# Kernel tuning notes

Measured on AMD Instinct MI355X. Metric: run time of the kernel, lower is better.

## Reference

```python
import jax, jax.numpy as jnp
import numpy as np

SOBEL_X = jnp.array([[-1., 0., 1.], [-2., 0., 2.], [-1., 0., 1.]], dtype=jnp.float32)
SOBEL_Y = jnp.array([[-1., -2., -1.], [0., 0., 0.], [1., 2., 1.]], dtype=jnp.float32)


def _dwconv(x, k):
    # depthwise 3x3 conv, padding=1, groups=C. x: [B,C,H,W], k: [3,3]
    C = x.shape[1]
    kern = jnp.broadcast_to(k[None, None], (C, 1, 3, 3)).astype(x.dtype)
    return jax.lax.conv_general_dilated(
        x, kern, window_strides=(1, 1), padding=((1, 1), (1, 1)),
        dimension_numbers=('NCHW', 'OIHW', 'NCHW'), feature_group_count=C)


def setup_inputs() -> dict:
    key = jax.random.key(0)
    k1, _ = jax.random.split(key)
    u = jax.random.normal(k1, (16, 3, 512, 512), dtype=jnp.float32)
    theta = jnp.ones((1,), dtype=jnp.float32)
    return {"u": u, "theta": theta}


def reference(u, theta):
    # first derivatives
    ux = _dwconv(u, SOBEL_X)
    uy = _dwconv(u, SOBEL_Y)
    # second derivatives
    uxx = _dwconv(ux, SOBEL_X)
    uxy = _dwconv(ux, SOBEL_Y)
    uyy = _dwconv(uy, SOBEL_Y)
    # Gaussian curvature
    denom = (1.0 + ux * ux + uy * uy) ** 2
    G = (uxx * uyy - uxy * uxy) / (denom + 1e-6)
    # theta * u is computed but unused in the original forward (kept faithful)
    _ = theta * u
    phi_G = jnp.exp(-jnp.abs(G))
    P = phi_G * ux
    Q = phi_G * uy
    div_term = _dwconv(P, SOBEL_X) + _dwconv(Q, SOBEL_Y)
    return u + div_term
```

## Files before the change

kernel.cpp:

```cpp
#include <hip/hip_runtime.h>
#include <math.h>


#define HB   8
#define NROW (HB + 6)
#define NT   256

#define STEP(TT, S0, S1, S2) do {                                              \
    const int Tt = (TT);                                                       \
               \
    const float ur0 = ucen[S0][0], ur1 = ucen[S0][1],                          \
                ur2 = ucen[S0][2], ur3 = ucen[S0][3];                          \
    if (Tt < NROW) {                                                           \
                        \
        const int gy = gy0 + Tt - 3;                                           \
        float* w = uw[S0];                                                     \
        if ((unsigned)gy < (unsigned)H) {                                      \
            const float* row = uc + (long)gy * W;                              \
            const float4 va = *(const float4*)(row + ca);                      \
            const float4 vb = *(const float4*)(row + c0);                      \
            const float4 vc = *(const float4*)(row + cc);                      \
            w[0] = inb0  ? va.x : 0.f;  w[1]  = inb1  ? va.y : 0.f;            \
            w[2] = inb2  ? va.z : 0.f;  w[3]  = inb3  ? va.w : 0.f;            \
            w[4] = vb.x;                w[5]  = vb.y;                          \
            w[6] = vb.z;                w[7]  = vb.w;                          \
            w[8] = inb8  ? vc.x : 0.f;  w[9]  = inb9  ? vc.y : 0.f;            \
            w[10] = inb10 ? vc.z : 0.f; w[11] = inb11 ? vc.w : 0.f;            \
        } else {                                                               \
            _Pragma("unroll") for (int i = 0; i < 12; ++i) w[i] = 0.f;         \
        }                                                                      \
        ucen[S0][0] = w[4]; ucen[S0][1] = w[5];                                \
        ucen[S0][2] = w[6]; ucen[S0][3] = w[7];                                \
    }                                                                          \
    if (Tt >= 2 && Tt < NROW) {                                                \
                 \
        float* xr = xw[S2]; float* yr = yw[S2];                                \
        const int gy = gy0 + Tt - 4;                                           \
        if ((unsigned)gy < (unsigned)H) {                                      \
            const float* a = uw[S1];                             \
            const float* m = uw[S2];                             \
            const float* b = uw[S0];                             \
            _Pragma("unroll") for (int c = 0; c < 8; ++c) {                    \
                const float A = a[c+1], B = a[c+2], C = a[c+3];                \
                const float D = m[c+1],             E = m[c+3];                \
                const float F = b[c+1], Gg = b[c+2], Hh = b[c+3];              \
                const float x = (C - A) + 2.f*(E - D) + (Hh - F);              \
                const float y = (F + 2.f*Gg + Hh) - (A + 2.f*B + C);           \
                xr[c] = mU[c+2] ? x : 0.f;                                     \
                yr[c] = mU[c+2] ? y : 0.f;                                     \
            }                                                                  \
        } else {                                                               \
            _Pragma("unroll") for (int c = 0; c < 8; ++c) { xr[c]=0.f; yr[c]=0.f; } \
        }                                                                      \
    }                                                                          \
    if (Tt >= 4 && Tt < NROW) {                                                \
                     \
        float* dp = dP[S1]; float* eq = eQ[S1];                                \
        const int gy = gy0 + Tt - 5;                                           \
        if ((unsigned)gy < (unsigned)H) {                                      \
            const float* xt = xw[S0];                         \
            const float* xm = xw[S1];                         \
            const float* xb = xw[S2];                         \
            const float* yt = yw[S0];                                          \
            const float* ym = yw[S1];                                          \
            const float* yb = yw[S2];                                          \
            float P[6], Q[6];                                                  \
            _Pragma("unroll") for (int c = 0; c < 6; ++c) {                    \
                const float xc = xm[c+1], yc = ym[c+1];                        \
                const float uxx = (xt[c+2]-xt[c]) + 2.f*(xm[c+2]-xm[c])        \
                                + (xb[c+2]-xb[c]);                             \
                const float uxy = (xb[c] + 2.f*xb[c+1] + xb[c+2])              \
                                - (xt[c] + 2.f*xt[c+1] + xt[c+2]);             \
                const float uyy = (yb[c] + 2.f*yb[c+1] + yb[c+2])              \
                                - (yt[c] + 2.f*yt[c+1] + yt[c+2]);             \
                const float den = 1.f + xc*xc + yc*yc;                         \
                const float Gv = (uxx*uyy - uxy*uxy)                           \
                               * __builtin_amdgcn_rcpf(den*den + 1e-6f);       \
                const float phi = __expf(-fabsf(Gv));                          \
                   \
                P[c] = phi * xc;                                               \
                Q[c] = phi * yc;                                               \
            }                                                                  \
            dp[0] = P[2]-P[0]; dp[1] = P[3]-P[1];                              \
            dp[2] = P[4]-P[2]; dp[3] = P[5]-P[3];                              \
            eq[0] = Q[0]+2.f*Q[1]+Q[2]; eq[1] = Q[1]+2.f*Q[2]+Q[3];            \
            eq[2] = Q[2]+2.f*Q[3]+Q[4]; eq[3] = Q[3]+2.f*Q[4]+Q[5];            \
        } else {                                                               \
            _Pragma("unroll") for (int c = 0; c < 4; ++c) { dp[c]=0.f; eq[c]=0.f; } \
        }                                                                      \
    }                                                                          \
    if (Tt >= 6 && Tt < NROW) {                                                \
         \
                  \
        const float o0 = ur0 + (dP[S2][0] + 2.f*dP[S0][0] + dP[S1][0])         \
                             + (eQ[S1][0] - eQ[S2][0]);                        \
        const float o1 = ur1 + (dP[S2][1] + 2.f*dP[S0][1] + dP[S1][1])         \
                             + (eQ[S1][1] - eQ[S2][1]);                        \
        const float o2 = ur2 + (dP[S2][2] + 2.f*dP[S0][2] + dP[S1][2])         \
                             + (eQ[S1][2] - eQ[S2][2]);                        \
        const float o3 = ur3 + (dP[S2][3] + 2.f*dP[S0][3] + dP[S1][3])         \
                             + (eQ[S1][3] - eQ[S2][3]);                        \
        *(float4*)(oc + (long)(gy0 + Tt - 6) * W + c0) =                       \
            make_float4(o0, o1, o2, o3);                                       \
    }                                                                          \
} while (0)

__global__ __launch_bounds__(NT) void gcdd_sweep(
    const float* __restrict__ u, float* __restrict__ out, int H, int W)
{
    const int tid   = threadIdx.x;
    const int strip = tid & 127;
    const int band  = tid >> 7;
    const int c0    = strip * 4;
    const int gy0   = (blockIdx.y * 2 + band) * HB;
    const long chan = blockIdx.z;
    const float* __restrict__ uc = u + chan * (long)H * W;
    float* __restrict__ oc = out + chan * (long)H * W;

    const int ca = (c0 - 4 < 0) ? 0 : (c0 - 4);
    const int cc = (c0 + 4 > W - 4) ? (W - 4) : (c0 + 4);

    bool mU[12];
    #pragma unroll
    for (int i = 0; i < 12; ++i)
        mU[i] = (unsigned)(c0 - 4 + i) < (unsigned)W;
    const bool inb0 = mU[0], inb1 = mU[1], inb2 = mU[2], inb3 = mU[3];
    const bool inb8 = mU[8], inb9 = mU[9], inb10 = mU[10], inb11 = mU[11];

    float uw[3][12];
    float ucen[3][4] = {};
    float xw[3][8], yw[3][8];
    float dP[3][4], eQ[3][4];

    for (int t = 0; t < NROW + 1; t += 3) {
        STEP(t + 0, 0, 1, 2);
        STEP(t + 1, 1, 2, 0);
        STEP(t + 2, 2, 0, 1);
    }
}

extern "C" void kernel_launch(void* const* d_in, const int* in_sizes, int n_in,
                              void* d_out, int out_size, void* d_ws, size_t ws_size,
                              hipStream_t stream) {
    const float* u = (const float*)d_in[0];
    float* out = (float*)d_out;

    const int H = 512, W = 512;
    const int channels = in_sizes[0] / (H * W);

    dim3 grid(1, H / (2 * HB), channels);
    dim3 block(NT);
    gcdd_sweep<<<grid, block, 0, stream>>>(u, out, H, W);
}
```

Measured before the change: 50.85 us.

## Cache separable horizontal partial sums per row and double band height

Each first-derivative row now stores its horizontal Sobel partial sums (differences and smoothed sums) once, so the second-derivative stage only combines three cached rows vertically instead of recomputing the horizontal stencil for all three rows. The band height doubles from 8 to 16 rows, which amortises the 6-row halo recompute over more output rows. The loop bound changes so the last STEP group still covers the larger row count. In exchange the kernel keeps more per-thread registers, which may lower occupancy, and there are half as many blocks.

```diff
diff --git a/kernel.cpp b/kernel.cpp
--- a/kernel.cpp
+++ b/kernel.cpp
@@ -2,7 +2,7 @@
 #include <math.h>
 
 
-#define HB   8
+#define HB   16
 #define NROW (HB + 6)
 #define NT   256
 
@@ -34,8 +34,8 @@
     }                                                                          \
     if (Tt >= 2 && Tt < NROW) {                                                \
                  \
-        float* xr = xw[S2]; float* yr = yw[S2];                                \
         const int gy = gy0 + Tt - 4;                                           \
+        float xr[8], yr[8];                                                    \
         if ((unsigned)gy < (unsigned)H) {                                      \
             const float* a = uw[S1];                             \
             const float* m = uw[S2];                             \
@@ -52,34 +52,34 @@
         } else {                                                               \
             _Pragma("unroll") for (int c = 0; c < 8; ++c) { xr[c]=0.f; yr[c]=0.f; } \
         }                                                                      \
+                                   \
+        _Pragma("unroll") for (int c = 0; c < 6; ++c) {                        \
+            Dx[S2][c] = xr[c+2] - xr[c];                                       \
+            Sx[S2][c] = xr[c] + 2.f*xr[c+1] + xr[c+2];                         \
+            Sy[S2][c] = yr[c] + 2.f*yr[c+1] + yr[c+2];                         \
+            xc[S2][c] = xr[c+1];                                               \
+            yc[S2][c] = yr[c+1];                                               \
+        }                                                                      \
     }                                                                          \
     if (Tt >= 4 && Tt < NROW) {                                                \
                      \
         float* dp = dP[S1]; float* eq = eQ[S1];                                \
         const int gy = gy0 + Tt - 5;                                           \
         if ((unsigned)gy < (unsigned)H) {                                      \
-            const float* xt = xw[S0];                         \
-            const float* xm = xw[S1];                         \
-            const float* xb = xw[S2];                         \
-            const float* yt = yw[S0];                                          \
-            const float* ym = yw[S1];                                          \
-            const float* yb = yw[S2];                                          \
+             \
             float P[6], Q[6];                                                  \
             _Pragma("unroll") for (int c = 0; c < 6; ++c) {                    \
-                const float xc = xm[c+1], yc = ym[c+1];                        \
-                const float uxx = (xt[c+2]-xt[c]) + 2.f*(xm[c+2]-xm[c])        \
-                                + (xb[c+2]-xb[c]);                             \
-                const float uxy = (xb[c] + 2.f*xb[c+1] + xb[c+2])              \
-                                - (xt[c] + 2.f*xt[c+1] + xt[c+2]);             \
-                const float uyy = (yb[c] + 2.f*yb[c+1] + yb[c+2])              \
-                                - (yt[c] + 2.f*yt[c+1] + yt[c+2]);             \
-                const float den = 1.f + xc*xc + yc*yc;                         \
+                const float xc_ = xc[S1][c], yc_ = yc[S1][c];                  \
+                const float uxx = Dx[S0][c] + 2.f*Dx[S1][c] + Dx[S2][c];       \
+                const float uxy = Sx[S2][c] - Sx[S0][c];                       \
+                const float uyy = Sy[S2][c] - Sy[S0][c];                       \
+                const float den = 1.f + xc_*xc_ + yc_*yc_;                     \
                 const float Gv = (uxx*uyy - uxy*uxy)                           \
                                * __builtin_amdgcn_rcpf(den*den + 1e-6f);       \
                 const float phi = __expf(-fabsf(Gv));                          \
-                   \
-                P[c] = phi * xc;                                               \
-                Q[c] = phi * yc;                                               \
+                 \
+                P[c] = phi * xc_;                                              \
+                Q[c] = phi * yc_;                                              \
             }                                                                  \
             dp[0] = P[2]-P[0]; dp[1] = P[3]-P[1];                              \
             dp[2] = P[4]-P[2]; dp[3] = P[5]-P[3];                              \
@@ -129,10 +129,10 @@
 
     float uw[3][12];
     float ucen[3][4] = {};
-    float xw[3][8], yw[3][8];
+    float Dx[3][6], Sx[3][6], Sy[3][6], xc[3][6], yc[3][6];
     float dP[3][4], eQ[3][4];
 
-    for (int t = 0; t < NROW + 1; t += 3) {
+    for (int t = 0; t < NROW + 2; t += 3) {
         STEP(t + 0, 0, 1, 2);
         STEP(t + 1, 1, 2, 0);
         STEP(t + 2, 2, 0, 1);
```

Result: no change. 50.91 us (+0.1%).
